# Kernel tuning notes

Hardware: AMD Instinct MI355X
Metric: run time of the kernel (lower is better)

The kernel has to match this reference:

```python
import jax, jax.numpy as jnp
import numpy as np

B, S, H = 2, 2048, 1024
NH, NKV, D = 16, 8, 128
EPS = 1e-6
THETA = 1000000.0


def _rope_tables():
    inv_freq = 1.0 / (THETA ** (np.arange(0, D, 2, dtype=np.float32) / D))  # [D/2]
    pos = np.arange(S, dtype=np.float32)
    freqs = np.outer(pos, inv_freq)                 # [S, D/2]
    emb = np.concatenate([freqs, freqs], axis=-1)   # [S, D]
    cos = np.broadcast_to(np.cos(emb), (B, S, D)).copy()
    sin = np.broadcast_to(np.sin(emb), (B, S, D)).copy()
    return jnp.asarray(cos), jnp.asarray(sin)


def setup_inputs() -> dict:
    key = jax.random.key(0)
    ks = jax.random.split(key, 6)
    cos, sin = _rope_tables()
    return {
        "hidden_states": jax.random.normal(ks[0], (B, S, H), jnp.float32),
        "cos": cos,
        "sin": sin,
        "Wq": jax.random.normal(ks[1], (NH * D, H), jnp.float32) * (H ** -0.5),
        "Wk": jax.random.normal(ks[2], (NKV * D, H), jnp.float32) * (H ** -0.5),
        "Wv": jax.random.normal(ks[3], (NKV * D, H), jnp.float32) * (H ** -0.5),
        "Wo": jax.random.normal(ks[4], (H, NH * D), jnp.float32) * ((NH * D) ** -0.5),
        "q_norm_w": jnp.ones((D,), jnp.float32),
        "k_norm_w": jnp.ones((D,), jnp.float32),
    }


def _rms_norm(x, w):
    # norm over last dim (head_dim), computed in fp32
    var = jnp.mean(x.astype(jnp.float32) ** 2, axis=-1, keepdims=True)
    return w * (x * jax.lax.rsqrt(var + EPS))


def _rotate_half(x):
    x1, x2 = jnp.split(x, 2, axis=-1)
    return jnp.concatenate([-x2, x1], axis=-1)


def reference(hidden_states, cos, sin, Wq, Wk, Wv, Wo, q_norm_w, k_norm_w):
    b, s, _ = hidden_states.shape
    # projections -> [B, n_heads, S, D]
    q = (hidden_states @ Wq.T).reshape(b, s, NH, D)
    k = (hidden_states @ Wk.T).reshape(b, s, NKV, D)
    v = (hidden_states @ Wv.T).reshape(b, s, NKV, D)
    q = _rms_norm(q, q_norm_w).transpose(0, 2, 1, 3)   # [B,NH,S,D]
    k = _rms_norm(k, k_norm_w).transpose(0, 2, 1, 3)   # [B,NKV,S,D]
    v = v.transpose(0, 2, 1, 3)                        # [B,NKV,S,D]
    # RoPE (cos/sin: [B,S,D] -> broadcast over heads)
    c = cos[:, None, :, :]
    sn = sin[:, None, :, :]
    q = q * c + _rotate_half(q) * sn
    k = k * c + _rotate_half(k) * sn
    # repeat_kv for GQA
    n_rep = NH // NKV
    k = jnp.repeat(k, n_rep, axis=1)                   # [B,NH,S,D]
    v = jnp.repeat(v, n_rep, axis=1)
    scale = D ** -0.5
    scores = jnp.einsum('bhqd,bhkd->bhqk', q, k) * scale
    causal = jnp.tril(jnp.ones((s, s), bool))
    scores = jnp.where(causal[None, None], scores, -jnp.inf)
    attn = jax.nn.softmax(scores.astype(jnp.float32), axis=-1)
    out = jnp.einsum('bhqk,bhkd->bhqd', attn, v)       # [B,NH,S,D]
    out = out.transpose(0, 2, 1, 3).reshape(b, s, NH * D)
    return out @ Wo.T                                  # [B,S,H]
```

## Files before the change

### kernel.cpp

```cpp
#include <hip/hip_runtime.h>
#include <hip/hip_bf16.h>
#include <stdint.h>

#define BB 2
#define SS 2048
#define HH 1024
#define NHEAD 16
#define NKVH 8
#define DD 128
#define MM (BB*SS)

typedef __bf16 bf16_t;
typedef __bf16 bf16x8 __attribute__((ext_vector_type(8)));
typedef __bf16 bf16x4 __attribute__((ext_vector_type(4)));
typedef float  f32x4  __attribute__((ext_vector_type(4)));

__global__ __launch_bounds__(256) void k_cvt_all(
    const float* __restrict__ h, const float* __restrict__ wq,
    const float* __restrict__ wk, const float* __restrict__ wv,
    const float* __restrict__ wo, bf16_t* __restrict__ hbf,
    bf16_t* __restrict__ wqkv, bf16_t* __restrict__ wob) {
  int i = blockIdx.x * 256 + threadIdx.x;
  const int stride = gridDim.x * 256;
  for (; i < 2621440; i += stride) {
    const float* src; bf16_t* dst; int off;
    if (i < 1048576)      { src = h;  dst = hbf;            off = i; }
    else if (i < 1572864) { src = wq; dst = wqkv;           off = i - 1048576; }
    else if (i < 1835008) { src = wk; dst = wqkv + 2097152; off = i - 1572864; }
    else if (i < 2097152) { src = wv; dst = wqkv + 3145728; off = i - 1835008; }
    else                  { src = wo; dst = wob;            off = i - 2097152; }
    float4 v = reinterpret_cast<const float4*>(src)[off];
    bf16x4 o;
    o[0] = (bf16_t)v.x; o[1] = (bf16_t)v.y; o[2] = (bf16_t)v.z; o[3] = (bf16_t)v.w;
    reinterpret_cast<bf16x4*>(dst)[off] = o;
  }
}

__global__ __launch_bounds__(256) void k_zero(float4* __restrict__ p, int n4) {
  int i = blockIdx.x * 256 + threadIdx.x;
  const int stride = gridDim.x * 256;
  const float4 z = make_float4(0.f, 0.f, 0.f, 0.f);
  for (; i < n4; i += stride) p[i] = z;
}

template <typename CT, int ATOM>
__global__ __launch_bounds__(256, 3) void k_gemm_lds(
    const bf16_t* __restrict__ A, const bf16_t* __restrict__ Bm,
    CT* __restrict__ C, int M, int N, int LD, int Ksplit) {
  __shared__ bf16_t As[128 * 64];
  __shared__ bf16_t Bs[128 * 64];
  const int t = threadIdx.x;
  const int lane = t & 63, wave = t >> 6;
  const int c = lane & 15, g = lane >> 4;
  const int wm = wave >> 1, wn = wave & 1;
  const long m0 = (long)blockIdx.y * 128;
  const long n0 = (long)blockIdx.x * 128;
  const long kbase = (long)blockIdx.z * Ksplit;
  const int srow = t >> 3, sc8 = t & 7;

  const bf16_t* Ag = A + (m0 + srow) * LD + kbase + sc8 * 8;
  const bf16_t* Bg = Bm + (n0 + srow) * LD + kbase + sc8 * 8;

  f32x4 acc[4][4] = {};
  const int nk = Ksplit >> 6;
  for (int kt = 0; kt < nk; ++kt) {
    const long koff = (long)kt * 64;
    __syncthreads();
#pragma unroll
    for (int i = 0; i < 4; ++i) {
      __builtin_amdgcn_global_load_lds(
          (const __attribute__((address_space(1))) uint32_t*)(const void*)(Ag + (long)i * 32 * LD + koff),
          (__attribute__((address_space(3))) uint32_t*)(void*)(&As[(i * 256 + t) * 8]),
          16, 0, 0);
      __builtin_amdgcn_global_load_lds(
          (const __attribute__((address_space(1))) uint32_t*)(const void*)(Bg + (long)i * 32 * LD + koff),
          (__attribute__((address_space(3))) uint32_t*)(void*)(&Bs[(i * 256 + t) * 8]),
          16, 0, 0);
    }
    __syncthreads();
#pragma unroll
    for (int kk = 0; kk < 2; ++kk) {
      bf16x8 af[4], bfr[4];
#pragma unroll
      for (int mi = 0; mi < 4; ++mi)
        af[mi] = *reinterpret_cast<const bf16x8*>(
            &As[(wm * 64 + mi * 16 + c) * 64 + kk * 32 + g * 8]);
#pragma unroll
      for (int ni = 0; ni < 4; ++ni)
        bfr[ni] = *reinterpret_cast<const bf16x8*>(
            &Bs[(wn * 64 + ni * 16 + c) * 64 + kk * 32 + g * 8]);
#pragma unroll
      for (int mi = 0; mi < 4; ++mi)
#pragma unroll
        for (int ni = 0; ni < 4; ++ni)
          acc[mi][ni] = __builtin_amdgcn_mfma_f32_16x16x32_bf16(
              af[mi], bfr[ni], acc[mi][ni], 0, 0, 0);
    }
  }
#pragma unroll
  for (int mi = 0; mi < 4; ++mi)
#pragma unroll
    for (int ni = 0; ni < 4; ++ni)
#pragma unroll
      for (int r = 0; r < 4; ++r) {
        long m = m0 + wm * 64 + mi * 16 + 4 * g + r;
        long n = n0 + wn * 64 + ni * 16 + c;
        if (ATOM) atomicAdd((float*)&C[m * N + n], acc[mi][ni][r]);
        else      C[m * N + n] = (CT)acc[mi][ni][r];
      }
}

__global__ __launch_bounds__(256) void k_nr(
    const bf16_t* __restrict__ raw, bf16_t* __restrict__ outp,
    const float* __restrict__ w, const float* __restrict__ cosb,
    const float* __restrict__ sinb, int nheads, int rstride) {
  const int wid = (blockIdx.x * 256 + threadIdx.x) >> 6;
  const int lane = threadIdx.x & 63;
  const int h = wid % nheads;
  const int bs = wid / nheads;
  const int b = bs / SS, s = bs - b * SS;
  const bf16_t* rp = raw + (long)bs * rstride + h * DD;
  float x0 = (float)rp[lane];
  float x1 = (float)rp[lane + 64];
  float ssq = x0 * x0 + x1 * x1;
#pragma unroll
  for (int m = 1; m < 64; m <<= 1) ssq += __shfl_xor(ssq, m);
  const float rs = rsqrtf(ssq * (1.0f / DD) + 1e-6f);
  const float xn0 = x0 * rs * w[lane];
  const float xn1 = x1 * rs * w[lane + 64];
  const float cc = cosb[(long)bs * DD + lane];
  const float sn = sinb[(long)bs * DD + lane];
  bf16_t o0 = (bf16_t)(xn0 * cc - xn1 * sn);
  bf16_t o1 = (bf16_t)(xn1 * cc + xn0 * sn);
  bf16_t* op = outp + (((long)b * nheads + h) * SS + s) * DD;
  op[lane] = o0;
  op[lane + 64] = o1;
}

__global__ __launch_bounds__(256) void k_vt(const bf16_t* __restrict__ src,
                                            bf16_t* __restrict__ vt) {
  __shared__ bf16_t Ls[64 * 136];
  const int t = threadIdx.x;
  const int s0 = blockIdx.x * 64;
  const int kvh = blockIdx.y;
  const int b = blockIdx.z;
  const bf16_t* ip = src + ((long)b * SS) * 4096 + 3072 + kvh * DD;
#pragma unroll
  for (int i = 0; i < 4; ++i) {
    const int cid = i * 256 + t;
    const int sr = cid >> 4, c8 = cid & 15;
    *reinterpret_cast<uint4*>(&Ls[sr * 136 + c8 * 8]) =
        *reinterpret_cast<const uint4*>(ip + (long)(s0 + sr) * 4096 + c8 * 8);
  }
  __syncthreads();
  const int d = t >> 1, sh = (t & 1) * 32;
  bf16_t* op = vt + (((long)b * NKVH + kvh) * DD + d) * SS + s0 + sh;
  bf16_t buf[32];
#pragma unroll
  for (int j = 0; j < 32; ++j) buf[j] = Ls[(sh + j) * 136 + d];
#pragma unroll
  for (int q = 0; q < 4; ++q)
    reinterpret_cast<uint4*>(op)[q] = reinterpret_cast<uint4*>(buf)[q];
}

__global__ __launch_bounds__(256, 2) void k_attn(
    const bf16_t* __restrict__ Qh, const bf16_t* __restrict__ Kh,
    const bf16_t* __restrict__ VT, bf16_t* __restrict__ AO) {
  __shared__ bf16_t Ks[64 * 128];
  __shared__ bf16_t Vs[128 * 64];
  __shared__ bf16_t Pq[4 * 2 * 16 * 64];
  const int t = threadIdx.x;
  const int lane = t & 63, wave = t >> 6;
  const int c = lane & 15, g = lane >> 4;

  const int id = blockIdx.x;
  const int xcd = id & 7, j2 = (id >> 3) & 3, qt8 = (id >> 5) & 7, half = id >> 8;
  const int qt = half ? (15 - qt8) : qt8;
  const int hb = xcd * 4 + j2;
  const int h = hb & 15, b = hb >> 4;
  const int kvh = h >> 1;

  const int qbase = qt * 128 + wave * 32;
  const int qg0 = qbase + c, qg1 = qbase + 16 + c;

  const bf16_t* qp = Qh + (((long)b * NHEAD + h) * SS) * DD;
  bf16x8 qf[2][4];
#pragma unroll
  for (int qc = 0; qc < 2; ++qc)
#pragma unroll
    for (int kb = 0; kb < 4; ++kb)
      qf[qc][kb] = *reinterpret_cast<const bf16x8*>(
          qp + (long)(qbase + qc * 16 + c) * DD + kb * 32 + g * 8);

  const bf16_t* kp = Kh + ((long)b * NKVH + kvh) * SS * DD;
  const bf16_t* vtp = VT + ((long)b * NKVH + kvh) * DD * SS;

  f32x4 o[8][2] = {};
  float mrow[2] = {-1e30f, -1e30f}, lrow[2] = {0.f, 0.f};
  const int srow2 = t >> 4, sc16 = t & 15;
  const int kv_end = qt * 128 + 128;
  const float scale = 0.08838834764831845f;
  const int c7x8 = 8 * (c & 7);

  for (int kv0 = 0; kv0 < kv_end; kv0 += 64) {
    __syncthreads();
#pragma unroll
    for (int rr = 0; rr < 4; ++rr) {
      const int row = srow2 + rr * 16;
      uint4 kvv = *reinterpret_cast<const uint4*>(kp + (long)(kv0 + row) * DD + sc16 * 8);
      *reinterpret_cast<uint4*>(&Ks[row * 128 + 8 * (sc16 ^ (row & 7))]) = kvv;
    }
#pragma unroll
    for (int i = 0; i < 4; ++i) {
      const int cid = i * 256 + t;
      const int d = cid >> 3, c8 = cid & 7;
      uint4 vv = *reinterpret_cast<const uint4*>(vtp + (long)d * SS + kv0 + c8 * 8);
      *reinterpret_cast<uint4*>(&Vs[d * 64 + 8 * (c8 ^ (d & 7))]) = vv;
    }
    __syncthreads();

    if (kv0 <= qbase + 31) {
      f32x4 s[2][4] = {};
#pragma unroll
      for (int kb = 0; kb < 4; ++kb) {
        bf16x8 kf[4];
#pragma unroll
        for (int kc = 0; kc < 4; ++kc)
          kf[kc] = *reinterpret_cast<const bf16x8*>(
              &Ks[(kc * 16 + c) * 128 + 8 * (((kb << 2) | g) ^ (c & 7))]);
#pragma unroll
        for (int qc = 0; qc < 2; ++qc)
#pragma unroll
          for (int kc = 0; kc < 4; ++kc)
            s[qc][kc] = __builtin_amdgcn_mfma_f32_16x16x32_bf16(
                kf[kc], qf[qc][kb], s[qc][kc], 0, 0, 0);
      }
#pragma unroll
      for (int qc = 0; qc < 2; ++qc) {
        const int qg = qc ? qg1 : qg0;
        float sv[16];
#pragma unroll
        for (int i = 0; i < 16; ++i) {
          const int key = kv0 + (i >> 2) * 16 + 4 * g + (i & 3);
          const float x = s[qc][i >> 2][i & 3];
          sv[i] = (key <= qg) ? x * scale : -1e30f;
        }
        float vm = sv[0];
#pragma unroll
        for (int i = 1; i < 16; ++i) vm = fmaxf(vm, sv[i]);
        vm = fmaxf(vm, __shfl_xor(vm, 16));
        vm = fmaxf(vm, __shfl_xor(vm, 32));
        const float mnew = fmaxf(mrow[qc], vm);
        const float alpha = __expf(mrow[qc] - mnew);
        float p[16], ps = 0.f;
#pragma unroll
        for (int i = 0; i < 16; ++i) { p[i] = __expf(sv[i] - mnew); ps += p[i]; }
        ps += __shfl_xor(ps, 16);
        ps += __shfl_xor(ps, 32);
        lrow[qc] = lrow[qc] * alpha + ps;
        mrow[qc] = mnew;
#pragma unroll
        for (int dt = 0; dt < 8; ++dt) o[dt][qc] = o[dt][qc] * alpha;
#pragma unroll
        for (int kc = 0; kc < 4; ++kc) {
          bf16x4 pk;
#pragma unroll
          for (int r = 0; r < 4; ++r) pk[r] = (bf16_t)p[kc * 4 + r];
          *reinterpret_cast<bf16x4*>(
              &Pq[((wave * 2 + qc) * 16 + c) * 64 + ((kc * 16 + 4 * g) ^ c7x8)]) = pk;
        }
      }
#pragma unroll
      for (int kc2 = 0; kc2 < 2; ++kc2) {
        bf16x8 pf[2];
#pragma unroll
        for (int qc = 0; qc < 2; ++qc)
          pf[qc] = *reinterpret_cast<const bf16x8*>(
              &Pq[((wave * 2 + qc) * 16 + c) * 64 + ((kc2 * 32 + g * 8) ^ c7x8)]);
#pragma unroll
        for (int dt = 0; dt < 8; ++dt) {
          const int dr = dt * 16 + c;
          bf16x8 vf = *reinterpret_cast<const bf16x8*>(
              &Vs[dr * 64 + 8 * ((kc2 * 4 + g) ^ (c & 7))]);
#pragma unroll
          for (int qc = 0; qc < 2; ++qc)
            o[dt][qc] = __builtin_amdgcn_mfma_f32_16x16x32_bf16(
                vf, pf[qc], o[dt][qc], 0, 0, 0);
        }
      }
    }
  }
#pragma unroll
  for (int qc = 0; qc < 2; ++qc) {
    const float linv = 1.0f / lrow[qc];
    bf16_t* aop = AO + ((long)(b * SS) + qbase + qc * 16 + c) * (NHEAD * DD) + h * DD;
#pragma unroll
    for (int dt = 0; dt < 8; ++dt) {
      bf16x4 ov;
#pragma unroll
      for (int r = 0; r < 4; ++r) ov[r] = (bf16_t)(o[dt][qc][r] * linv);
      *reinterpret_cast<bf16x4*>(aop + dt * 16 + 4 * g) = ov;
    }
  }
}

extern "C" void kernel_launch(void* const* d_in, const int* in_sizes, int n_in,
                              void* d_out, int out_size, void* d_ws, size_t ws_size,
                              hipStream_t stream) {
  const float* hidden = (const float*)d_in[0];
  const float* cosb   = (const float*)d_in[1];
  const float* sinb   = (const float*)d_in[2];
  const float* Wq     = (const float*)d_in[3];
  const float* Wk     = (const float*)d_in[4];
  const float* Wv     = (const float*)d_in[5];
  const float* Wo     = (const float*)d_in[6];
  const float* qnw    = (const float*)d_in[7];
  const float* knw    = (const float*)d_in[8];
  float* outp = (float*)d_out;
  char* ws = (char*)d_ws;
  const size_t MB = 1024 * 1024;
  bf16_t* hbf   = (bf16_t*)(ws + 0);
  bf16_t* wqkv  = (bf16_t*)(ws + 8 * MB);
  bf16_t* wob   = (bf16_t*)(ws + 16 * MB);
  bf16_t* qkvr  = (bf16_t*)(ws + 20 * MB);
  bf16_t* qn    = (bf16_t*)(ws + 52 * MB);
  bf16_t* kn    = (bf16_t*)(ws + 68 * MB);
  bf16_t* vt    = (bf16_t*)(ws + 76 * MB);
  bf16_t* ao    = qkvr;

  k_cvt_all<<<2048, 256, 0, stream>>>(hidden, Wq, Wk, Wv, Wo, hbf, wqkv, wob);

  k_gemm_lds<bf16_t, 0><<<dim3(32, 32, 1), 256, 0, stream>>>(
      hbf, wqkv, qkvr, MM, 4096, 1024, 1024);

  k_nr<<<MM * NHEAD / 4, 256, 0, stream>>>(qkvr, qn, qnw, cosb, sinb, NHEAD, 4096);
  k_nr<<<MM * NKVH / 4, 256, 0, stream>>>(qkvr + 2048, kn, knw, cosb, sinb, NKVH, 4096);
  k_vt<<<dim3(32, 8, 2), 256, 0, stream>>>(qkvr, vt);

  k_attn<<<dim3(512), 256, 0, stream>>>(qn, kn, vt, ao);

  k_zero<<<1024, 256, 0, stream>>>((float4*)outp, MM * 1024 / 4);
  k_gemm_lds<float, 1><<<dim3(8, 32, 2), 256, 0, stream>>>(
      ao, wob, outp, MM, 1024, 2048, 1024);
}
```

Measured before the change: 348.9 us.

## Drop split-K atomics for output GEMM and tile V-transpose into contiguous blocks

```diff
diff --git a/kernel.cpp b/kernel.cpp
--- a/kernel.cpp
+++ b/kernel.cpp
@@ -36,17 +36,10 @@
   }
 }
 
-__global__ __launch_bounds__(256) void k_zero(float4* __restrict__ p, int n4) {
-  int i = blockIdx.x * 256 + threadIdx.x;
-  const int stride = gridDim.x * 256;
-  const float4 z = make_float4(0.f, 0.f, 0.f, 0.f);
-  for (; i < n4; i += stride) p[i] = z;
-}
-
-template <typename CT, int ATOM>
+template <typename CT>
 __global__ __launch_bounds__(256, 3) void k_gemm_lds(
     const bf16_t* __restrict__ A, const bf16_t* __restrict__ Bm,
-    CT* __restrict__ C, int M, int N, int LD, int Ksplit) {
+    CT* __restrict__ C, int M, int N, int LD) {
   __shared__ bf16_t As[128 * 64];
   __shared__ bf16_t Bs[128 * 64];
   const int t = threadIdx.x;
@@ -55,14 +48,13 @@
   const int wm = wave >> 1, wn = wave & 1;
   const long m0 = (long)blockIdx.y * 128;
   const long n0 = (long)blockIdx.x * 128;
-  const long kbase = (long)blockIdx.z * Ksplit;
   const int srow = t >> 3, sc8 = t & 7;
 
-  const bf16_t* Ag = A + (m0 + srow) * LD + kbase + sc8 * 8;
-  const bf16_t* Bg = Bm + (n0 + srow) * LD + kbase + sc8 * 8;
+  const bf16_t* Ag = A + (m0 + srow) * LD + sc8 * 8;
+  const bf16_t* Bg = Bm + (n0 + srow) * LD + sc8 * 8;
 
   f32x4 acc[4][4] = {};
-  const int nk = Ksplit >> 6;
+  const int nk = LD >> 6;
   for (int kt = 0; kt < nk; ++kt) {
     const long koff = (long)kt * 64;
     __syncthreads();
@@ -105,8 +97,7 @@
       for (int r = 0; r < 4; ++r) {
         long m = m0 + wm * 64 + mi * 16 + 4 * g + r;
         long n = n0 + wn * 64 + ni * 16 + c;
-        if (ATOM) atomicAdd((float*)&C[m * N + n], acc[mi][ni][r]);
-        else      C[m * N + n] = (CT)acc[mi][ni][r];
+        C[m * N + n] = (CT)acc[mi][ni][r];
       }
 }
 
@@ -154,7 +145,7 @@
   }
   __syncthreads();
   const int d = t >> 1, sh = (t & 1) * 32;
-  bf16_t* op = vt + (((long)b * NKVH + kvh) * DD + d) * SS + s0 + sh;
+  bf16_t* op = vt + (((long)b * NKVH + kvh) * 32 + (s0 >> 6)) * 8192 + d * 64 + sh;
   bf16_t buf[32];
 #pragma unroll
   for (int j = 0; j < 32; ++j) buf[j] = Ls[(sh + j) * 136 + d];
@@ -193,7 +184,7 @@
           qp + (long)(qbase + qc * 16 + c) * DD + kb * 32 + g * 8);
 
   const bf16_t* kp = Kh + ((long)b * NKVH + kvh) * SS * DD;
-  const bf16_t* vtp = VT + ((long)b * NKVH + kvh) * DD * SS;
+  const bf16_t* vtp = VT + ((long)b * NKVH + kvh) * 32 * 8192;
 
   f32x4 o[8][2] = {};
   float mrow[2] = {-1e30f, -1e30f}, lrow[2] = {0.f, 0.f};
@@ -210,12 +201,15 @@
       uint4 kvv = *reinterpret_cast<const uint4*>(kp + (long)(kv0 + row) * DD + sc16 * 8);
       *reinterpret_cast<uint4*>(&Ks[row * 128 + 8 * (sc16 ^ (row & 7))]) = kvv;
     }
-#pragma unroll
-    for (int i = 0; i < 4; ++i) {
-      const int cid = i * 256 + t;
-      const int d = cid >> 3, c8 = cid & 7;
-      uint4 vv = *reinterpret_cast<const uint4*>(vtp + (long)d * SS + kv0 + c8 * 8);
-      *reinterpret_cast<uint4*>(&Vs[d * 64 + 8 * (c8 ^ (d & 7))]) = vv;
+    {
+      const bf16_t* tb = vtp + (kv0 >> 6) * 8192;
+#pragma unroll
+      for (int i = 0; i < 4; ++i) {
+        const int cid = i * 256 + t;
+        const int d = cid >> 3, c8 = cid & 7;
+        uint4 vv = *reinterpret_cast<const uint4*>(tb + cid * 8);
+        *reinterpret_cast<uint4*>(&Vs[d * 64 + 8 * (c8 ^ (d & 7))]) = vv;
+      }
     }
     __syncthreads();
 
@@ -330,8 +324,7 @@
 
   k_cvt_all<<<2048, 256, 0, stream>>>(hidden, Wq, Wk, Wv, Wo, hbf, wqkv, wob);
 
-  k_gemm_lds<bf16_t, 0><<<dim3(32, 32, 1), 256, 0, stream>>>(
-      hbf, wqkv, qkvr, MM, 4096, 1024, 1024);
+  k_gemm_lds<bf16_t><<<dim3(32, 32), 256, 0, stream>>>(hbf, wqkv, qkvr, MM, 4096, 1024);
 
   k_nr<<<MM * NHEAD / 4, 256, 0, stream>>>(qkvr, qn, qnw, cosb, sinb, NHEAD, 4096);
   k_nr<<<MM * NKVH / 4, 256, 0, stream>>>(qkvr + 2048, kn, knw, cosb, sinb, NKVH, 4096);
@@ -339,7 +332,5 @@
 
   k_attn<<<dim3(512), 256, 0, stream>>>(qn, kn, vt, ao);
 
-  k_zero<<<1024, 256, 0, stream>>>((float4*)outp, MM * 1024 / 4);
-  k_gemm_lds<float, 1><<<dim3(8, 32, 2), 256, 0, stream>>>(
-      ao, wob, outp, MM, 1024, 2048, 1024);
-}
+  k_gemm_lds<float><<<dim3(8, 32), 256, 0, stream>>>(ao, wob, outp, MM, 1024, 2048);
+}
```

Result: faster. 335.7 us (-3.8%).
